# Kernel tuning notes

Measured on AMD Instinct MI355X. Metric: run time of the kernel, lower is better.

The kernel has to match this reference:

```python
import jax, jax.numpy as jnp
import numpy as np

DIM, HID, SEQ = 768, 2048, 4096
LR, MOM, WD, THRESH = 1e-3, 0.9, 0.01, 0.1


def _net(p, x):
    W1, b1, W2, b2, W3, b3, W4, b4 = p
    h = jax.nn.relu(x @ W1 + b1)
    h = jax.nn.relu(h @ W2 + b2)
    h = jax.nn.relu(h @ W3 + b3)
    return h @ W4 + b4


def _loss(p, t):
    # t: [dim]; token.unsqueeze(0) then mse_loss (mean over all elements)
    pred = _net(p, t[None, :])
    return jnp.mean((pred - t[None, :]) ** 2)


def _ttt(params, x):
    toks = x[::4]  # `if i % 4 != 0: continue`

    def step(carry, t):
        p, buf, inited = carry
        g = jax.grad(_loss)(p, t)
        surprise = sum(jnp.linalg.norm(gi) for gi in jax.tree_util.tree_leaves(g))
        # momentum buffer: first observation initializes it
        buf_new = jnp.where(inited, MOM * buf + (1.0 - MOM) * surprise, surprise)

        def upd(q):
            qd = jax.tree_util.tree_map(lambda w: w * (1.0 - WD), q)  # weight decay
            g2 = jax.grad(_loss)(qd, t)                                # fresh fwd/bwd
            return jax.tree_util.tree_map(lambda w, gi: w - LR * gi, qd, g2)  # SGD step

        p_new = jax.lax.cond(buf_new > THRESH, upd, lambda q: q, p)
        return (p_new, buf_new, jnp.bool_(True)), None

    (pf, _, _), _ = jax.lax.scan(step, (params, jnp.float32(0.0), jnp.bool_(False)), toks)
    return pf


def setup_inputs() -> dict:
    key = jax.random.key(0)
    ks = jax.random.split(key, 5)

    def lin(k, fi, fo):
        kw, kb = jax.random.split(k)
        w = jax.random.normal(kw, (fi, fo), jnp.float32) / np.sqrt(fi).astype(np.float32)
        b = jax.random.normal(kb, (fo,), jnp.float32) * 0.01
        return w, b

    W1, b1 = lin(ks[0], DIM, HID)
    W2, b2 = lin(ks[1], HID, HID)
    W3, b3 = lin(ks[2], HID, HID)
    W4, b4 = lin(ks[3], HID, DIM)
    x = jax.random.normal(ks[4], (SEQ, DIM), jnp.float32)
    return dict(x=x, W1=W1, b1=b1, W2=W2, b2=b2, W3=W3, b3=b3, W4=W4, b4=b4, do_ttt=1)


def reference(x, W1, b1, W2, b2, W3, b3, W4, b4, do_ttt):
    params = (W1, b1, W2, b2, W3, b3, W4, b4)
    if do_ttt:
        params = _ttt(params, x)
    out = _net(params, x)            # eval pass over full sequence
    return out.mean(axis=0, keepdims=True)  # memory_summary [1, dim]
```

## Files before the change

### kernel.cpp

```cpp
#include <hip/hip_runtime.h>
#include <cstddef>

#define LRC 0.001f
#define DEC 0.99f

typedef float vf4 __attribute__((ext_vector_type(4)));

static const size_t OFF_Z1T  = 0;
static const size_t OFF_Z2TP = 65536;
static const size_t OFF_Z2TQ = 131072;
static const size_t OFF_Z3TP = 196608;
static const size_t OFF_Z3TQ = 262144;
static const size_t OFF_Z4TP = 327680;
static const size_t OFF_Z4TQ = 352256;
static const size_t OFF_H1F = 376832;
static const size_t OFF_H1Q = 378880;
static const size_t OFF_H2F = 380928;
static const size_t OFF_H2Q = 382976;
static const size_t OFF_H3F = 385024;
static const size_t OFF_H3Q0 = 387072;
static const size_t OFF_D4F = 389120;
static const size_t OFF_D4Q = 389888;
static const size_t OFF_D3F = 390656;
static const size_t OFF_D3Q = 392704;
static const size_t OFF_D2F = 394752;
static const size_t OFF_D2Q = 396800;
static const size_t OFF_D1F = 398848;
static const size_t OFF_D1Q = 400896;
static const size_t OFF_NSQ = 402944;
static const size_t OFF_SL3 = 402960;
static const size_t OFF_SL2 = 403216;
static const size_t OFF_SL1 = 403472;
static const size_t OFF_BUF = 403728;
static const size_t OFF_CONDF = 403730;
static const size_t OFF_MSUM = 403732;
static const size_t OFF_HA  = 428308;
static const size_t OFF_BAR = OFF_HA;
static const size_t OFF_H3Q1 = OFF_HA + 1024;
static const size_t OFF_HB  = 2525460;

struct V8 { vf4 v[8]; };

__device__ __forceinline__ float ld_cv(const float* p) {
    float v;
    asm volatile("global_load_dword %0, %1, off sc0 sc1\n\ts_waitcnt vmcnt(0)"
                 : "=&v"(v) : "v"(p) : "memory");
    return v;
}
__device__ __forceinline__ vf4 ld4_cv(const float* p) {
    vf4 v;
    asm volatile("global_load_dwordx4 %0, %1, off sc0 sc1\n\ts_waitcnt vmcnt(0)"
                 : "=&v"(v) : "v"(p) : "memory");
    return v;
}
__device__ __forceinline__ V8 ld32_cv(const float* p) {
    V8 r;
    asm volatile(
        "global_load_dwordx4 %0, %8, off sc0 sc1\n\t"
        "global_load_dwordx4 %1, %8, off offset:16 sc0 sc1\n\t"
        "global_load_dwordx4 %2, %8, off offset:32 sc0 sc1\n\t"
        "global_load_dwordx4 %3, %8, off offset:48 sc0 sc1\n\t"
        "global_load_dwordx4 %4, %8, off offset:64 sc0 sc1\n\t"
        "global_load_dwordx4 %5, %8, off offset:80 sc0 sc1\n\t"
        "global_load_dwordx4 %6, %8, off offset:96 sc0 sc1\n\t"
        "global_load_dwordx4 %7, %8, off offset:112 sc0 sc1\n\t"
        "s_waitcnt vmcnt(0)"
        : "=&v"(r.v[0]), "=&v"(r.v[1]), "=&v"(r.v[2]), "=&v"(r.v[3]),
          "=&v"(r.v[4]), "=&v"(r.v[5]), "=&v"(r.v[6]), "=&v"(r.v[7])
        : "v"(p) : "memory");
    return r;
}
__device__ __forceinline__ V8 ldrow_cv(const float* p) {
    const float* q = p + 1024;
    V8 r;
    asm volatile(
        "global_load_dwordx4 %0, %8, off sc0 sc1\n\t"
        "global_load_dwordx4 %1, %8, off offset:1024 sc0 sc1\n\t"
        "global_load_dwordx4 %2, %8, off offset:2048 sc0 sc1\n\t"
        "global_load_dwordx4 %3, %8, off offset:3072 sc0 sc1\n\t"
        "global_load_dwordx4 %4, %9, off sc0 sc1\n\t"
        "global_load_dwordx4 %5, %9, off offset:1024 sc0 sc1\n\t"
        "global_load_dwordx4 %6, %9, off offset:2048 sc0 sc1\n\t"
        "global_load_dwordx4 %7, %9, off offset:3072 sc0 sc1\n\t"
        "s_waitcnt vmcnt(0)"
        : "=&v"(r.v[0]), "=&v"(r.v[1]), "=&v"(r.v[2]), "=&v"(r.v[3]),
          "=&v"(r.v[4]), "=&v"(r.v[5]), "=&v"(r.v[6]), "=&v"(r.v[7])
        : "v"(p), "v"(q) : "memory");
    return r;
}
__device__ __forceinline__ void ldrow3_cv(const float* p, vf4& a, vf4& b, vf4& c) {
    asm volatile(
        "global_load_dwordx4 %0, %3, off sc0 sc1\n\t"
        "global_load_dwordx4 %1, %3, off offset:1024 sc0 sc1\n\t"
        "global_load_dwordx4 %2, %3, off offset:2048 sc0 sc1\n\t"
        "s_waitcnt vmcnt(0)"
        : "=&v"(a), "=&v"(b), "=&v"(c) : "v"(p) : "memory");
}
__device__ __forceinline__ void st_cv(float* p, float v) {
    asm volatile("global_store_dword %0, %1, off sc0 sc1" :: "v"(p), "v"(v) : "memory");
}
__device__ __forceinline__ void st_cv4(float* p, vf4 v) {
    asm volatile("global_store_dwordx4 %0, %1, off sc0 sc1" :: "v"(p), "v"(v) : "memory");
}
__device__ __forceinline__ float sum32(const V8& z) {
    float s = 0.f;
#pragma unroll
    for (int i = 0; i < 8; ++i) s += z.v[i].x + z.v[i].y + z.v[i].z + z.v[i].w;
    return s;
}

__device__ float block_reduce_512(float v) {
    __shared__ float red[512];
    int t = threadIdx.x;
    red[t] = v;
    __syncthreads();
    for (int s = 256; s > 0; s >>= 1) {
        if (t < s) red[t] += red[t + s];
        __syncthreads();
    }
    float r = red[0];
    __syncthreads();
    return r;
}

__device__ inline void gbar(int* bar, int bi) {
    asm volatile("s_waitcnt vmcnt(0) lgkmcnt(0)" ::: "memory");
    __syncthreads();
    if (threadIdx.x == 0) {
        int target = bi * 16 + 15;
        int g = (int)(blockIdx.x >> 4);
        int v = __hip_atomic_fetch_add(&bar[g * 16], 1, __ATOMIC_RELAXED, __HIP_MEMORY_SCOPE_AGENT);
        if (v == target) {
            int r = __hip_atomic_fetch_add(&bar[260], 1, __ATOMIC_RELAXED, __HIP_MEMORY_SCOPE_AGENT);
            if (r == target)
                __hip_atomic_store(&bar[276], bi + 1, __ATOMIC_RELAXED, __HIP_MEMORY_SCOPE_AGENT);
        }
        while (__hip_atomic_load(&bar[276], __ATOMIC_RELAXED, __HIP_MEMORY_SCOPE_AGENT) <= bi)
            __builtin_amdgcn_s_sleep(8);
    }
    __syncthreads();
}

__device__ __forceinline__ void fwd2phase(int bblk, int tid, int w, int lane, vf4* s4,
        const float* zinTP, const float* zinTQ, const float* bin,
        float* W, int Nout, float* zoutTP, float* zoutTQ,
        const float* uprev, const float* vprev, float* bl, bool upd) {
    float* sm = (float*)s4;
    float* hs = sm + 4096; float* hq = sm + 4160; float* us = sm + 4224;
    int p = bblk & 31, g = bblk >> 5;
    if (tid < 64) {
        int k = p * 64 + tid;
        V8 zp = ld32_cv(zinTP + (size_t)k * 32);
        float ssum = sum32(zp);
        float bv = ld_cv(bin + k);
        float h = fmaxf(ssum + bv, 0.f);
        float hqq;
        if (zinTQ) {
            V8 zq = ld32_cv(zinTQ + (size_t)k * 32);
            hqq = fmaxf(DEC * (sum32(zq) + bv), 0.f);
        } else {
            hqq = DEC * h;
        }
        hs[tid] = h; hq[tid] = hqq;
        us[tid] = upd ? (LRC * ld_cv(uprev + k)) : 0.f;
    }
    __syncthreads();
    int c0 = g * 256 + lane * 4;
    vf4 vpv = {0.f, 0.f, 0.f, 0.f};
    if (upd) vpv = ld4_cv(vprev + c0);
    vf4 ap = {0.f, 0.f, 0.f, 0.f};
    vf4 aq = {0.f, 0.f, 0.f, 0.f};
    if (upd) {
#pragma unroll
        for (int r = 0; r < 8; ++r) {
            int kk = w * 8 + r;
            float* wp = W + (size_t)(p * 64 + kk) * Nout + c0;
            vf4 wv = *(const vf4*)wp;
            wv = DEC * wv - us[kk] * vpv;
            st_cv4(wp, wv);
            ap += hs[kk] * wv; aq += hq[kk] * wv;
        }
    } else {
#pragma unroll
        for (int r = 0; r < 8; ++r) {
            int kk = w * 8 + r;
            const vf4 wv = *(const vf4*)(W + (size_t)(p * 64 + kk) * Nout + c0);
            ap += hs[kk] * wv; aq += hq[kk] * wv;
        }
    }
    if (upd && bblk == 0) {
        int c = tid * 4;
        if (c < Nout) {
            vf4 dq = ld4_cv(vprev + c);
            vf4 bv = ld4_cv(bl + c);
            st_cv4(bl + c, DEC * bv - LRC * dq);
        }
    }
    s4[w * 64 + lane] = ap;
    s4[512 + w * 64 + lane] = aq;
    __syncthreads();
    if (w == 0) {
        vf4 sp = s4[lane], sq4 = s4[512 + lane];
#pragma unroll
        for (int q = 1; q < 8; ++q) {
            sp += s4[q * 64 + lane];
            sq4 += s4[512 + q * 64 + lane];
        }
        st_cv(zoutTP + (size_t)(c0 + 0) * 32 + p, sp.x);
        st_cv(zoutTP + (size_t)(c0 + 1) * 32 + p, sp.y);
        st_cv(zoutTP + (size_t)(c0 + 2) * 32 + p, sp.z);
        st_cv(zoutTP + (size_t)(c0 + 3) * 32 + p, sp.w);
        st_cv(zoutTQ + (size_t)(c0 + 0) * 32 + p, sq4.x);
        st_cv(zoutTQ + (size_t)(c0 + 1) * 32 + p, sq4.y);
        st_cv(zoutTQ + (size_t)(c0 + 2) * 32 + p, sq4.z);
        st_cv(zoutTQ + (size_t)(c0 + 3) * 32 + p, sq4.w);
    }
}

__device__ __forceinline__ void bwdphase(int bblk, int tid, int w, int lane,
        float* sm, float* sqw, const float* W,
        const float* dinP, const float* dinQ,
        const float* hP, const float* hQ,
        float* doutP, float* doutQ, float* slot) {
    float* dsP = sm; float* dsQ = sm + 2048;
    {
        int k4 = tid * 4;
        vf4 vP = ld4_cv(dinP + k4);
        vf4 vQ = ld4_cv(dinQ + k4);
        *(vf4*)(dsP + k4) = vP;
        *(vf4*)(dsQ + k4) = vQ;
    }
    __syncthreads();
    int j = bblk * 8 + w;
    V8 r = ldrow_cv(W + (size_t)j * 2048 + lane * 4);
    float ap = 0.f, aq = 0.f;
#pragma unroll
    for (int i = 0; i < 8; ++i) {
        int k0 = lane * 4 + i * 256;
        vf4 wv = r.v[i];
        ap += wv.x * dsP[k0] + wv.y * dsP[k0 + 1] + wv.z * dsP[k0 + 2] + wv.w * dsP[k0 + 3];
        aq += wv.x * dsQ[k0] + wv.y * dsQ[k0 + 1] + wv.z * dsQ[k0 + 2] + wv.w * dsQ[k0 + 3];
    }
#pragma unroll
    for (int off = 32; off > 0; off >>= 1) {
        ap += __shfl_down(ap, off);
        aq += __shfl_down(aq, off);
    }
    if (lane == 0) {
        float dp = (ld_cv(hP + j) > 0.f) ? ap : 0.f;
        float dq = (ld_cv(hQ + j) > 0.f) ? DEC * aq : 0.f;
        st_cv(doutP + j, dp); st_cv(doutQ + j, dq); sqw[w] = dp * dp;
    }
    __syncthreads();
    if (tid == 0) {
        float t = 0.f;
#pragma unroll
        for (int q = 0; q < 8; ++q) t += sqw[q];
        st_cv(slot + bblk, t);
    }
}

__global__ __launch_bounds__(512) void k_ttt(const float* __restrict__ x,
        float* __restrict__ W1, float* __restrict__ b1,
        float* __restrict__ W2, float* __restrict__ b2,
        float* __restrict__ W3, float* __restrict__ b3,
        float* __restrict__ W4, float* __restrict__ b4,
        float* __restrict__ wsf, const int* __restrict__ flag, int* __restrict__ bar) {
    if (*flag == 0) return;
    const int b = blockIdx.x, tid = threadIdx.x;
    const int w = tid >> 6, lane = tid & 63;
    __shared__ vf4 s4[1408];
    __shared__ float cnd[12];
    __shared__ float sqw[8];
    __shared__ float updsh;
    float* sm = (float*)s4;
    int bi = 0;

    for (int s = 0; s < 1024; ++s) {
        const float* xt = x + (size_t)s * 3072;
        const float* xp = x + (size_t)(s > 0 ? s - 1 : 0) * 3072;
        float* h3q_cur = wsf + ((s & 1) ? OFF_H3Q1 : OFF_H3Q0);
        const float* h3q_prev = wsf + ((s & 1) ? OFF_H3Q0 : OFF_H3Q1);

        {
            int g = b >> 5, p = b & 31;
            int c0 = g * 256 + lane * 4;
            int kb = p * 24 + w * 3;
            vf4 wv0 = *(const vf4*)(W1 + (size_t)(kb + 0) * 2048 + c0);
            vf4 wv1 = *(const vf4*)(W1 + (size_t)(kb + 1) * 2048 + c0);
            vf4 wv2 = *(const vf4*)(W1 + (size_t)(kb + 2) * 2048 + c0);
            float a0 = xt[kb + 0], a1 = xt[kb + 1], a2 = xt[kb + 2];
            vf4 dv = {0.f, 0.f, 0.f, 0.f};
            float u0 = 0.f, u1 = 0.f, u2 = 0.f;
            float cond = 0.f;
            if (s > 0) {
                dv = ld4_cv(wsf + OFF_D1Q + c0);
                u0 = LRC * xp[kb + 0]; u1 = LRC * xp[kb + 1]; u2 = LRC * xp[kb + 2];
                if (w < 3) {
                    const float* sl = wsf + (w == 0 ? OFF_SL1 : (w == 1 ? OFF_SL2 : OFF_SL3));
                    vf4 v4 = ld4_cv(sl + lane * 4);
                    float v = v4.x + v4.y + v4.z + v4.w;
#pragma unroll
                    for (int off = 32; off > 0; off >>= 1) v += __shfl_down(v, off);
                    if (lane == 0) cnd[w] = v;
                } else if (w == 3 && lane < 6) {
                    cnd[3 + lane] = (lane < 5) ? ld_cv(wsf + OFF_NSQ + lane)
                                               : ld_cv(wsf + OFF_BUF + ((s - 1) & 1));
                }
                __syncthreads();
                float nd1 = sqrtf(cnd[0]), nd2 = sqrtf(cnd[1]), nd3 = sqrtf(cnd[2]);
                float nx = sqrtf(cnd[3]), nh1 = sqrtf(cnd[4]), nh2 = sqrtf(cnd[5]);
                float nh3 = sqrtf(cnd[6]), nd4 = sqrtf(cnd[7]);
                float bufold = cnd[8];
                float surprise = nx * nd1 + nd1 + nh1 * nd2 + nd2 + nh2 * nd3 + nd3 + nh3 * nd4 + nd4;
                float bufnew = (s == 1) ? surprise : (0.9f * bufold + 0.1f * surprise);
                cond = (bufnew > 0.1f) ? 1.f : 0.f;
                if (b == 0 && tid == 0) {
                    st_cv(wsf + OFF_BUF + (s & 1), bufnew);
                    st_cv(wsf + OFF_CONDF, cond);
                }
            } else {
                if (b == 0 && tid == 0) st_cv(wsf + OFF_CONDF, 0.f);
            }
            if (tid == 0) updsh = cond;
            if (cond != 0.f) {
                wv0 = DEC * wv0 - u0 * dv;
                wv1 = DEC * wv1 - u1 * dv;
                wv2 = DEC * wv2 - u2 * dv;
                st_cv4(W1 + (size_t)(kb + 0) * 2048 + c0, wv0);
                st_cv4(W1 + (size_t)(kb + 1) * 2048 + c0, wv1);
                st_cv4(W1 + (size_t)(kb + 2) * 2048 + c0, wv2);
                if (b == 0) {
                    int c = tid * 4;
                    vf4 dq = ld4_cv(wsf + OFF_D1Q + c);
                    vf4 bv = ld4_cv(b1 + c);
                    st_cv4(b1 + c, DEC * bv - LRC * dq);
                }
            }
            vf4 acc = a0 * wv0 + a1 * wv1 + a2 * wv2;
            s4[w * 64 + lane] = acc;
            __syncthreads();
            if (w == 0) {
                vf4 t = s4[lane];
#pragma unroll
                for (int q = 1; q < 8; ++q) t += s4[q * 64 + lane];
                st_cv(wsf + OFF_Z1T + (size_t)(c0 + 0) * 32 + p, t.x);
                st_cv(wsf + OFF_Z1T + (size_t)(c0 + 1) * 32 + p, t.y);
                st_cv(wsf + OFF_Z1T + (size_t)(c0 + 2) * 32 + p, t.z);
                st_cv(wsf + OFF_Z1T + (size_t)(c0 + 3) * 32 + p, t.w);
            }
        }
        gbar(bar, bi++);

        bool upd = (updsh != 0.f);

        fwd2phase(b, tid, w, lane, s4, wsf + OFF_Z1T, nullptr, b1, W2, 2048,
                  wsf + OFF_Z2TP, wsf + OFF_Z2TQ, wsf + OFF_H1Q, wsf + OFF_D2Q, b2, upd);
        gbar(bar, bi++);

        fwd2phase(b, tid, w, lane, s4, wsf + OFF_Z2TP, wsf + OFF_Z2TQ, b2, W3, 2048,
                  wsf + OFF_Z3TP, wsf + OFF_Z3TQ, wsf + OFF_H2Q, wsf + OFF_D3Q, b3, upd);
        gbar(bar, bi++);

        if (b < 96) {
            fwd2phase(b, tid, w, lane, s4, wsf + OFF_Z3TP, wsf + OFF_Z3TQ, b3, W4, 768,
                      wsf + OFF_Z4TP, wsf + OFF_Z4TQ, h3q_prev, wsf + OFF_D4Q, b4, upd);
        } else {
            int idx = b - 96;
            if (idx < 16) {
                if (tid < 128) {
                    int e = idx * 128 + tid;
                    V8 z = ld32_cv(wsf + OFF_Z1T + (size_t)e * 32);
                    float h = fmaxf(sum32(z) + ld_cv(b1 + e), 0.f);
                    st_cv(wsf + OFF_H1F + e, h);
                    st_cv(wsf + OFF_H1Q + e, DEC * h);
                }
            } else if (idx < 32) {
                if (tid < 128) {
                    int e = (idx - 16) * 128 + tid;
                    V8 zp = ld32_cv(wsf + OFF_Z2TP + (size_t)e * 32);
                    V8 zq = ld32_cv(wsf + OFF_Z2TQ + (size_t)e * 32);
                    float bv = ld_cv(b2 + e);
                    st_cv(wsf + OFF_H2F + e, fmaxf(sum32(zp) + bv, 0.f));
                    st_cv(wsf + OFF_H2Q + e, fmaxf(DEC * (sum32(zq) + bv), 0.f));
                }
            } else if (idx < 48) {
                if (tid < 128) {
                    int e = (idx - 32) * 128 + tid;
                    V8 zp = ld32_cv(wsf + OFF_Z3TP + (size_t)e * 32);
                    V8 zq = ld32_cv(wsf + OFF_Z3TQ + (size_t)e * 32);
                    float bv = ld_cv(b3 + e);
                    st_cv(wsf + OFF_H3F + e, fmaxf(sum32(zp) + bv, 0.f));
                    st_cv(h3q_cur + e, fmaxf(DEC * (sum32(zq) + bv), 0.f));
                }
            } else if (idx == 48) {
                float v = 0.f;
                for (int e = tid; e < 768; e += 512) { float xv = xt[e]; v += xv * xv; }
                float t = block_reduce_512(v);
                if (tid == 0) st_cv(wsf + OFF_NSQ + 0, t);
            } else if (idx == 49) {
                float v = 0.f;
                for (int e = tid; e < 2048; e += 512) {
                    V8 z = ld32_cv(wsf + OFF_Z1T + (size_t)e * 32);
                    float h = fmaxf(sum32(z) + ld_cv(b1 + e), 0.f);
                    v += h * h;
                }
                float t = block_reduce_512(v);
                if (tid == 0) st_cv(wsf + OFF_NSQ + 1, t);
            } else if (idx == 50) {
                float v = 0.f;
                for (int e = tid; e < 2048; e += 512) {
                    V8 z = ld32_cv(wsf + OFF_Z2TP + (size_t)e * 32);
                    float h = fmaxf(sum32(z) + ld_cv(b2 + e), 0.f);
                    v += h * h;
                }
                float t = block_reduce_512(v);
                if (tid == 0) st_cv(wsf + OFF_NSQ + 2, t);
            } else if (idx == 51) {
                float v = 0.f;
                for (int e = tid; e < 2048; e += 512) {
                    V8 z = ld32_cv(wsf + OFF_Z3TP + (size_t)e * 32);
                    float h = fmaxf(sum32(z) + ld_cv(b3 + e), 0.f);
                    v += h * h;
                }
                float t = block_reduce_512(v);
                if (tid == 0) st_cv(wsf + OFF_NSQ + 3, t);
            }
        }
        gbar(bar, bi++);

        {
            float* d4P = sm; float* d4Q = sm + 768;
            for (int e = tid; e < 768; e += 512) {
                V8 zp = ld32_cv(wsf + OFF_Z4TP + (size_t)e * 32);
                V8 zq = ld32_cv(wsf + OFF_Z4TQ + (size_t)e * 32);
                float bv = ld_cv(b4 + e), tv = xt[e];
                d4P[e] = 2.f * ((sum32(zp) + bv) - tv) * (1.f / 768.f);
                d4Q[e] = 2.f * (DEC * (sum32(zq) + bv) - tv) * (1.f / 768.f);
            }
            __syncthreads();
            int j = b * 8 + w;
            vf4 r0, r1, r2;
            ldrow3_cv(W4 + (size_t)j * 768 + lane * 4, r0, r1, r2);
            float ap = 0.f, aq = 0.f;
            {
                int k0 = lane * 4;
                ap += r0.x * d4P[k0] + r0.y * d4P[k0 + 1] + r0.z * d4P[k0 + 2] + r0.w * d4P[k0 + 3];
                aq += r0.x * d4Q[k0] + r0.y * d4Q[k0 + 1] + r0.z * d4Q[k0 + 2] + r0.w * d4Q[k0 + 3];
                k0 += 256;
                ap += r1.x * d4P[k0] + r1.y * d4P[k0 + 1] + r1.z * d4P[k0 + 2] + r1.w * d4P[k0 + 3];
                aq += r1.x * d4Q[k0] + r1.y * d4Q[k0 + 1] + r1.z * d4Q[k0 + 2] + r1.w * d4Q[k0 + 3];
                k0 += 256;
                ap += r2.x * d4P[k0] + r2.y * d4P[k0 + 1] + r2.z * d4P[k0 + 2] + r2.w * d4P[k0 + 3];
                aq += r2.x * d4Q[k0] + r2.y * d4Q[k0 + 1] + r2.z * d4Q[k0 + 2] + r2.w * d4Q[k0 + 3];
            }
#pragma unroll
            for (int off = 32; off > 0; off >>= 1) {
                ap += __shfl_down(ap, off);
                aq += __shfl_down(aq, off);
            }
            if (lane == 0) {
                float dp = (ld_cv(wsf + OFF_H3F + j) > 0.f) ? ap : 0.f;
                float dq = (ld_cv(h3q_cur + j) > 0.f) ? DEC * aq : 0.f;
                st_cv(wsf + OFF_D3F + j, dp); st_cv(wsf + OFF_D3Q + j, dq); sqw[w] = dp * dp;
            }
            __syncthreads();
            if (tid == 0) {
                float t = 0.f;
#pragma unroll
                for (int q = 0; q < 8; ++q) t += sqw[q];
                st_cv(wsf + OFF_SL3 + b, t);
            }
            if (b == 0) {
                float v = 0.f;
                for (int e = tid; e < 768; e += 512) {
                    st_cv(wsf + OFF_D4F + e, d4P[e]);
                    st_cv(wsf + OFF_D4Q + e, d4Q[e]);
                    v += d4P[e] * d4P[e];
                }
                float t = block_reduce_512(v);
                if (tid == 0) st_cv(wsf + OFF_NSQ + 4, t);
            }
        }
        gbar(bar, bi++);

        bwdphase(b, tid, w, lane, sm, sqw, W3,
                 wsf + OFF_D3F, wsf + OFF_D3Q, wsf + OFF_H2F, wsf + OFF_H2Q,
                 wsf + OFF_D2F, wsf + OFF_D2Q, wsf + OFF_SL2);
        gbar(bar, bi++);

        bwdphase(b, tid, w, lane, sm, sqw, W2,
                 wsf + OFF_D2F, wsf + OFF_D2Q, wsf + OFF_H1F, wsf + OFF_H1Q,
                 wsf + OFF_D1F, wsf + OFF_D1Q, wsf + OFF_SL1);
        gbar(bar, bi++);
    }
}

__global__ __launch_bounds__(512) void k_upd(int step, float* __restrict__ wsf,
                                             float* __restrict__ W1, float* __restrict__ b1,
                                             float* __restrict__ W2, float* __restrict__ b2,
                                             float* __restrict__ W3, float* __restrict__ b3,
                                             float* __restrict__ W4, float* __restrict__ b4,
                                             const float* __restrict__ xt,
                                             const int* __restrict__ flag) {
    if (*flag == 0) return;
    int tid = threadIdx.x, b = blockIdx.x;
    float s3 = block_reduce_512((tid < 256) ? wsf[OFF_SL3 + tid] : 0.f);
    float s2 = block_reduce_512((tid < 256) ? wsf[OFF_SL2 + tid] : 0.f);
    float s1 = block_reduce_512((tid < 256) ? wsf[OFF_SL1 + tid] : 0.f);
    __shared__ float condsh;
    if (tid == 0) {
        float nx = sqrtf(wsf[OFF_NSQ + 0]);
        float nh1 = sqrtf(wsf[OFF_NSQ + 1]);
        float nh2 = sqrtf(wsf[OFF_NSQ + 2]);
        float nh3 = sqrtf(wsf[OFF_NSQ + 3]);
        float nd4 = sqrtf(wsf[OFF_NSQ + 4]);
        float nd3 = sqrtf(s3), nd2 = sqrtf(s2), nd1 = sqrtf(s1);
        float surprise = nx * nd1 + nd1 + nh1 * nd2 + nd2 + nh2 * nd3 + nd3 + nh3 * nd4 + nd4;
        float bufold = wsf[OFF_BUF + (step & 1)];
        float bufnew = (step == 0) ? surprise : (0.9f * bufold + 0.1f * surprise);
        condsh = (bufnew > 0.1f) ? 1.f : 0.f;
    }
    __syncthreads();
    if (condsh == 0.f) return;

    const float* d1q = wsf + OFF_D1Q;
    const float* d2q = wsf + OFF_D2Q;
    const float* d3q = wsf + OFF_D3Q;
    const float* d4q = wsf + OFF_D4Q;
    const float* h1q = wsf + OFF_H1Q;
    const float* h2q = wsf + OFF_H2Q;
    const float* h3q = wsf + OFF_H3Q1;
    int c = tid * 4;
    {
        float4 dv = *(const float4*)(d1q + c);
#pragma unroll
        for (int r = 0; r < 3; ++r) {
            int i = b * 3 + r;
            float u = LRC * xt[i];
            float4* wp = (float4*)(W1 + (size_t)i * 2048 + c);
            float4 wv = *wp;
            wv.x = DEC * wv.x - u * dv.x; wv.y = DEC * wv.y - u * dv.y;
            wv.z = DEC * wv.z - u * dv.z; wv.w = DEC * wv.w - u * dv.w;
            *wp = wv;
        }
    }
    {
        float4 dv = *(const float4*)(d2q + c);
#pragma unroll
        for (int r = 0; r < 8; ++r) {
            int i = b * 8 + r;
            float u = LRC * h1q[i];
            float4* wp = (float4*)(W2 + (size_t)i * 2048 + c);
            float4 wv = *wp;
            wv.x = DEC * wv.x - u * dv.x; wv.y = DEC * wv.y - u * dv.y;
            wv.z = DEC * wv.z - u * dv.z; wv.w = DEC * wv.w - u * dv.w;
            *wp = wv;
        }
    }
    {
        float4 dv = *(const float4*)(d3q + c);
#pragma unroll
        for (int r = 0; r < 8; ++r) {
            int i = b * 8 + r;
            float u = LRC * h2q[i];
            float4* wp = (float4*)(W3 + (size_t)i * 2048 + c);
            float4 wv = *wp;
            wv.x = DEC * wv.x - u * dv.x; wv.y = DEC * wv.y - u * dv.y;
            wv.z = DEC * wv.z - u * dv.z; wv.w = DEC * wv.w - u * dv.w;
            *wp = wv;
        }
    }
    if (tid < 192) {
        float4 dv = *(const float4*)(d4q + c);
#pragma unroll
        for (int r = 0; r < 8; ++r) {
            int i = b * 8 + r;
            float u = LRC * h3q[i];
            float4* wp = (float4*)(W4 + (size_t)i * 768 + c);
            float4 wv = *wp;
            wv.x = DEC * wv.x - u * dv.x; wv.y = DEC * wv.y - u * dv.y;
            wv.z = DEC * wv.z - u * dv.z; wv.w = DEC * wv.w - u * dv.w;
            *wp = wv;
        }
    }
    if (b == 0) {
        float4 dv = *(const float4*)(d1q + c);
        float4* bp = (float4*)(b1 + c);
        float4 bv = *bp;
        bv.x = DEC * bv.x - LRC * dv.x; bv.y = DEC * bv.y - LRC * dv.y;
        bv.z = DEC * bv.z - LRC * dv.z; bv.w = DEC * bv.w - LRC * dv.w;
        *bp = bv;
    } else if (b == 1) {
        float4 dv = *(const float4*)(d2q + c);
        float4* bp = (float4*)(b2 + c);
        float4 bv = *bp;
        bv.x = DEC * bv.x - LRC * dv.x; bv.y = DEC * bv.y - LRC * dv.y;
        bv.z = DEC * bv.z - LRC * dv.z; bv.w = DEC * bv.w - LRC * dv.w;
        *bp = bv;
    } else if (b == 2) {
        float4 dv = *(const float4*)(d3q + c);
        float4* bp = (float4*)(b3 + c);
        float4 bv = *bp;
        bv.x = DEC * bv.x - LRC * dv.x; bv.y = DEC * bv.y - LRC * dv.y;
        bv.z = DEC * bv.z - LRC * dv.z; bv.w = DEC * bv.w - LRC * dv.w;
        *bp = bv;
    } else if (b == 3 && tid < 192) {
        float4 dv = *(const float4*)(d4q + c);
        float4* bp = (float4*)(b4 + c);
        float4 bv = *bp;
        bv.x = DEC * bv.x - LRC * dv.x; bv.y = DEC * bv.y - LRC * dv.y;
        bv.z = DEC * bv.z - LRC * dv.z; bv.w = DEC * bv.w - LRC * dv.w;
        *bp = bv;
    }
}

__global__ __launch_bounds__(256) void k_gemm(const float* __restrict__ A,
                                              const float* __restrict__ W,
                                              const float* __restrict__ bias,
                                              float* __restrict__ C,
                                              int M, int N, int K, int do_relu) {
    __shared__ float sA[16][64];
    __shared__ float sB[16][128];
    int bn = blockIdx.x, bm = blockIdx.y;
    int m0 = bm * 64, n0 = bn * 128;
    int tid = threadIdx.x;
    int tx = tid & 31, ty = tid >> 5;
    float acc[8][4];
#pragma unroll
    for (int i = 0; i < 8; ++i)
#pragma unroll
        for (int j = 0; j < 4; ++j) acc[i][j] = 0.f;

    for (int kt = 0; kt < K; kt += 16) {
        {
            int r = tid >> 2, cc = (tid & 3) * 4;
            const float4 a4 = *(const float4*)(A + (size_t)(m0 + r) * K + kt + cc);
            sA[cc + 0][r] = a4.x; sA[cc + 1][r] = a4.y; sA[cc + 2][r] = a4.z; sA[cc + 3][r] = a4.w;
        }
        {
            int r = tid >> 5, cc = (tid & 31) * 4;
            *(float4*)(&sB[r][cc]) = *(const float4*)(W + (size_t)(kt + r) * N + n0 + cc);
            *(float4*)(&sB[r + 8][cc]) = *(const float4*)(W + (size_t)(kt + r + 8) * N + n0 + cc);
        }
        __syncthreads();
#pragma unroll
        for (int k = 0; k < 16; ++k) {
            float av[8];
#pragma unroll
            for (int i = 0; i < 8; ++i) av[i] = sA[k][ty * 8 + i];
            float bx = sB[k][tx * 4 + 0], by = sB[k][tx * 4 + 1];
            float bz = sB[k][tx * 4 + 2], bw = sB[k][tx * 4 + 3];
#pragma unroll
            for (int i = 0; i < 8; ++i) {
                acc[i][0] += av[i] * bx; acc[i][1] += av[i] * by;
                acc[i][2] += av[i] * bz; acc[i][3] += av[i] * bw;
            }
        }
        __syncthreads();
    }
    float bx = bias[n0 + tx * 4 + 0], by = bias[n0 + tx * 4 + 1];
    float bz = bias[n0 + tx * 4 + 2], bw = bias[n0 + tx * 4 + 3];
#pragma unroll
    for (int i = 0; i < 8; ++i) {
        int m = m0 + ty * 8 + i;
        float4 v;
        v.x = acc[i][0] + bx; v.y = acc[i][1] + by;
        v.z = acc[i][2] + bz; v.w = acc[i][3] + bw;
        if (do_relu) {
            v.x = fmaxf(v.x, 0.f); v.y = fmaxf(v.y, 0.f);
            v.z = fmaxf(v.z, 0.f); v.w = fmaxf(v.w, 0.f);
        }
        *(float4*)(C + (size_t)m * N + n0 + tx * 4) = v;
    }
}

__global__ __launch_bounds__(128) void k_colsum(const float* __restrict__ Y,
                                                float* __restrict__ out) {
    int c = blockIdx.x * 128 + threadIdx.x;
    int r0 = blockIdx.y * 128;
    float s = 0.f;
    for (int r = 0; r < 128; ++r) s += Y[(size_t)(r0 + r) * 768 + c];
    out[blockIdx.y * 768 + c] = s;
}

__global__ __launch_bounds__(768) void k_out(const float* __restrict__ msum,
                                             float* __restrict__ out) {
    int c = threadIdx.x;
    float s = 0.f;
#pragma unroll
    for (int i = 0; i < 32; ++i) s += msum[i * 768 + c];
    out[c] = s * (1.f / 4096.f);
}

extern "C" void kernel_launch(void* const* d_in, const int* in_sizes, int n_in,
                              void* d_out, int out_size, void* d_ws, size_t ws_size,
                              hipStream_t stream) {
    const float* x = (const float*)d_in[0];
    float* W1 = (float*)d_in[1];
    float* b1 = (float*)d_in[2];
    float* W2 = (float*)d_in[3];
    float* b2 = (float*)d_in[4];
    float* W3 = (float*)d_in[5];
    float* b3 = (float*)d_in[6];
    float* W4 = (float*)d_in[7];
    float* b4 = (float*)d_in[8];
    const int* flag = (const int*)d_in[9];
    float* wsf = (float*)d_ws;
    int* bar = (int*)(wsf + OFF_BAR);

    hipMemsetAsync((void*)bar, 0, 1024 * sizeof(int), stream);

    void* args[] = {(void*)&x, (void*)&W1, (void*)&b1, (void*)&W2, (void*)&b2,
                    (void*)&W3, (void*)&b3, (void*)&W4, (void*)&b4,
                    (void*)&wsf, (void*)&flag, (void*)&bar};
    hipLaunchCooperativeKernel((void*)k_ttt, dim3(256), dim3(512), args, 0, stream);

    k_upd<<<256, 512, 0, stream>>>(1023, wsf, W1, b1, W2, b2, W3, b3, W4, b4,
                                   x + (size_t)1023 * 4 * 768, flag);

    float* HA = wsf + OFF_HA;
    float* HB = wsf + OFF_HB;
    for (int ch = 0; ch < 4; ++ch) {
        const float* Xc = x + (size_t)ch * 1024 * 768;
        k_gemm<<<dim3(16, 16), 256, 0, stream>>>(Xc, W1, b1, HA, 1024, 2048, 768, 1);
        k_gemm<<<dim3(16, 16), 256, 0, stream>>>(HA, W2, b2, HB, 1024, 2048, 2048, 1);
        k_gemm<<<dim3(16, 16), 256, 0, stream>>>(HB, W3, b3, HA, 1024, 2048, 2048, 1);
        k_gemm<<<dim3(6, 16), 256, 0, stream>>>(HA, W4, b4, HB, 1024, 768, 2048, 0);
        k_colsum<<<dim3(6, 8), 128, 0, stream>>>(HB, wsf + OFF_MSUM + (size_t)ch * 8 * 768);
    }
    k_out<<<1, 768, 0, stream>>>(wsf + OFF_MSUM, (float*)d_out);
}
```

Baseline: 72.48 ms.

## Batch coherent loads under one wait and spread z-transpose reductions across threads

Splits the coherent load helpers into issue and wait parts, so each phase issues all of its global loads together and then waits once, instead of waiting on every load in turn. The per-element 32-wide partial-sum reads of the transposed activations are spread across 8 (or 4) threads per element, with the reduction finished in shared memory, rather than one thread reading 32 floats serially. Also shortens the spin-barrier sleep and adds a two-blocks-per-CU launch bound. This trades larger shared memory use and extra syncthreads for more memory-level parallelism in the latency-bound persistent kernel.

```diff
diff --git a/kernel.cpp b/kernel.cpp
--- a/kernel.cpp
+++ b/kernel.cpp
@@ -39,40 +39,26 @@
 static const size_t OFF_H3Q1 = OFF_HA + 1024;
 static const size_t OFF_HB  = 2525460;
 
-struct V8 { vf4 v[8]; };
-
+#define PIN(v) asm volatile("" : "+v"(v))
+__device__ __forceinline__ void vmwait() { asm volatile("s_waitcnt vmcnt(0)" ::: "memory"); }
+__device__ __forceinline__ float ld_nw(const float* p) {
+    float v;
+    asm volatile("global_load_dword %0, %1, off sc0 sc1" : "=&v"(v) : "v"(p) : "memory");
+    return v;
+}
+__device__ __forceinline__ vf4 ld4_nw(const float* p) {
+    vf4 v;
+    asm volatile("global_load_dwordx4 %0, %1, off sc0 sc1" : "=&v"(v) : "v"(p) : "memory");
+    return v;
+}
 __device__ __forceinline__ float ld_cv(const float* p) {
-    float v;
-    asm volatile("global_load_dword %0, %1, off sc0 sc1\n\ts_waitcnt vmcnt(0)"
-                 : "=&v"(v) : "v"(p) : "memory");
-    return v;
+    float v = ld_nw(p); vmwait(); PIN(v); return v;
 }
 __device__ __forceinline__ vf4 ld4_cv(const float* p) {
-    vf4 v;
-    asm volatile("global_load_dwordx4 %0, %1, off sc0 sc1\n\ts_waitcnt vmcnt(0)"
-                 : "=&v"(v) : "v"(p) : "memory");
-    return v;
-}
-__device__ __forceinline__ V8 ld32_cv(const float* p) {
-    V8 r;
-    asm volatile(
-        "global_load_dwordx4 %0, %8, off sc0 sc1\n\t"
-        "global_load_dwordx4 %1, %8, off offset:16 sc0 sc1\n\t"
-        "global_load_dwordx4 %2, %8, off offset:32 sc0 sc1\n\t"
-        "global_load_dwordx4 %3, %8, off offset:48 sc0 sc1\n\t"
-        "global_load_dwordx4 %4, %8, off offset:64 sc0 sc1\n\t"
-        "global_load_dwordx4 %5, %8, off offset:80 sc0 sc1\n\t"
-        "global_load_dwordx4 %6, %8, off offset:96 sc0 sc1\n\t"
-        "global_load_dwordx4 %7, %8, off offset:112 sc0 sc1\n\t"
-        "s_waitcnt vmcnt(0)"
-        : "=&v"(r.v[0]), "=&v"(r.v[1]), "=&v"(r.v[2]), "=&v"(r.v[3]),
-          "=&v"(r.v[4]), "=&v"(r.v[5]), "=&v"(r.v[6]), "=&v"(r.v[7])
-        : "v"(p) : "memory");
-    return r;
-}
-__device__ __forceinline__ V8 ldrow_cv(const float* p) {
+    vf4 v = ld4_nw(p); vmwait(); PIN(v); return v;
+}
+__device__ __forceinline__ void ldrow_nw(const float* p, vf4* r) {
     const float* q = p + 1024;
-    V8 r;
     asm volatile(
         "global_load_dwordx4 %0, %8, off sc0 sc1\n\t"
         "global_load_dwordx4 %1, %8, off offset:1024 sc0 sc1\n\t"
@@ -81,19 +67,16 @@
         "global_load_dwordx4 %4, %9, off sc0 sc1\n\t"
         "global_load_dwordx4 %5, %9, off offset:1024 sc0 sc1\n\t"
         "global_load_dwordx4 %6, %9, off offset:2048 sc0 sc1\n\t"
-        "global_load_dwordx4 %7, %9, off offset:3072 sc0 sc1\n\t"
-        "s_waitcnt vmcnt(0)"
-        : "=&v"(r.v[0]), "=&v"(r.v[1]), "=&v"(r.v[2]), "=&v"(r.v[3]),
-          "=&v"(r.v[4]), "=&v"(r.v[5]), "=&v"(r.v[6]), "=&v"(r.v[7])
+        "global_load_dwordx4 %7, %9, off offset:3072 sc0 sc1"
+        : "=&v"(r[0]), "=&v"(r[1]), "=&v"(r[2]), "=&v"(r[3]),
+          "=&v"(r[4]), "=&v"(r[5]), "=&v"(r[6]), "=&v"(r[7])
         : "v"(p), "v"(q) : "memory");
-    return r;
-}
-__device__ __forceinline__ void ldrow3_cv(const float* p, vf4& a, vf4& b, vf4& c) {
+}
+__device__ __forceinline__ void ldrow3_nw(const float* p, vf4& a, vf4& b, vf4& c) {
     asm volatile(
         "global_load_dwordx4 %0, %3, off sc0 sc1\n\t"
         "global_load_dwordx4 %1, %3, off offset:1024 sc0 sc1\n\t"
-        "global_load_dwordx4 %2, %3, off offset:2048 sc0 sc1\n\t"
-        "s_waitcnt vmcnt(0)"
+        "global_load_dwordx4 %2, %3, off offset:2048 sc0 sc1"
         : "=&v"(a), "=&v"(b), "=&v"(c) : "v"(p) : "memory");
 }
 __device__ __forceinline__ void st_cv(float* p, float v) {
@@ -102,12 +85,7 @@
 __device__ __forceinline__ void st_cv4(float* p, vf4 v) {
     asm volatile("global_store_dwordx4 %0, %1, off sc0 sc1" :: "v"(p), "v"(v) : "memory");
 }
-__device__ __forceinline__ float sum32(const V8& z) {
-    float s = 0.f;
-#pragma unroll
-    for (int i = 0; i < 8; ++i) s += z.v[i].x + z.v[i].y + z.v[i].z + z.v[i].w;
-    return s;
-}
+__device__ __forceinline__ float sum4(vf4 v) { return v.x + v.y + v.z + v.w; }
 
 __device__ float block_reduce_512(float v) {
     __shared__ float red[512];
@@ -136,56 +114,82 @@
                 __hip_atomic_store(&bar[276], bi + 1, __ATOMIC_RELAXED, __HIP_MEMORY_SCOPE_AGENT);
         }
         while (__hip_atomic_load(&bar[276], __ATOMIC_RELAXED, __HIP_MEMORY_SCOPE_AGENT) <= bi)
-            __builtin_amdgcn_s_sleep(8);
-    }
-    __syncthreads();
-}
-
-__device__ __forceinline__ void fwd2phase(int bblk, int tid, int w, int lane, vf4* s4,
+            __builtin_amdgcn_s_sleep(4);
+    }
+    __syncthreads();
+}
+
+__device__ __forceinline__ void fwd2phase(int bblk, int tid, int w, int lane, float* SM,
         const float* zinTP, const float* zinTQ, const float* bin,
         float* W, int Nout, float* zoutTP, float* zoutTQ,
         const float* uprev, const float* vprev, float* bl, bool upd) {
-    float* sm = (float*)s4;
-    float* hs = sm + 4096; float* hq = sm + 4160; float* us = sm + 4224;
+    vf4* s4 = (vf4*)SM;
+    float* hP8   = SM + 6144;
+    float* hQ8   = SM + 6656;
+    float* biasL = SM + 7168;
+    float* usL   = SM + 7232;
+    float* hsL   = SM + 7296;
+    float* hqL   = SM + 7360;
     int p = bblk & 31, g = bblk >> 5;
+    int kb = p * 64;
+    int kk = tid >> 3, ch = tid & 7;
+    int c0 = g * 256 + lane * 4;
+    bool hasQ = (zinTQ != nullptr);
+
+    vf4 zp = ld4_nw(zinTP + (size_t)(kb + kk) * 32 + ch * 4);
+    vf4 zq;
+    if (hasQ) zq = ld4_nw(zinTQ + (size_t)(kb + kk) * 32 + ch * 4);
+    vf4 bi4; if (tid < 16) bi4 = ld4_nw(bin + kb + tid * 4);
+    vf4 uu4; if (upd && tid >= 16 && tid < 32) uu4 = ld4_nw(uprev + kb + (tid - 16) * 4);
+    vf4 vpv; if (upd) vpv = ld4_nw(vprev + c0);
+    vmwait();
+    PIN(zp); if (hasQ) PIN(zq);
+    if (tid < 16) PIN(bi4);
+    if (upd && tid >= 16 && tid < 32) PIN(uu4);
+    if (upd) PIN(vpv);
+
+    hP8[kk * 8 + ch] = sum4(zp);
+    if (hasQ) hQ8[kk * 8 + ch] = sum4(zq);
+    if (tid < 16) *(vf4*)(biasL + tid * 4) = bi4;
+    if (upd && tid >= 16 && tid < 32) *(vf4*)(usL + (tid - 16) * 4) = LRC * uu4;
+    __syncthreads();
     if (tid < 64) {
-        int k = p * 64 + tid;
-        V8 zp = ld32_cv(zinTP + (size_t)k * 32);
-        float ssum = sum32(zp);
-        float bv = ld_cv(bin + k);
-        float h = fmaxf(ssum + bv, 0.f);
-        float hqq;
-        if (zinTQ) {
-            V8 zq = ld32_cv(zinTQ + (size_t)k * 32);
-            hqq = fmaxf(DEC * (sum32(zq) + bv), 0.f);
+        float s = 0.f;
+#pragma unroll
+        for (int c = 0; c < 8; ++c) s += hP8[tid * 8 + c];
+        float bv = biasL[tid];
+        float h = fmaxf(s + bv, 0.f);
+        float hq;
+        if (hasQ) {
+            float sq = 0.f;
+#pragma unroll
+            for (int c = 0; c < 8; ++c) sq += hQ8[tid * 8 + c];
+            hq = fmaxf(DEC * (sq + bv), 0.f);
         } else {
-            hqq = DEC * h;
-        }
-        hs[tid] = h; hq[tid] = hqq;
-        us[tid] = upd ? (LRC * ld_cv(uprev + k)) : 0.f;
-    }
-    __syncthreads();
-    int c0 = g * 256 + lane * 4;
-    vf4 vpv = {0.f, 0.f, 0.f, 0.f};
-    if (upd) vpv = ld4_cv(vprev + c0);
+            hq = DEC * h;
+        }
+        hsL[tid] = h; hqL[tid] = hq;
+    }
+    __syncthreads();
+
     vf4 ap = {0.f, 0.f, 0.f, 0.f};
     vf4 aq = {0.f, 0.f, 0.f, 0.f};
     if (upd) {
 #pragma unroll
         for (int r = 0; r < 8; ++r) {
-            int kk = w * 8 + r;
-            float* wp = W + (size_t)(p * 64 + kk) * Nout + c0;
+            int k2 = w * 8 + r;
+            float* wp = W + (size_t)(p * 64 + k2) * Nout + c0;
             vf4 wv = *(const vf4*)wp;
-            wv = DEC * wv - us[kk] * vpv;
+            wv = DEC * wv - usL[k2] * vpv;
             st_cv4(wp, wv);
-            ap += hs[kk] * wv; aq += hq[kk] * wv;
+            ap += hsL[k2] * wv; aq += hqL[k2] * wv;
         }
     } else {
 #pragma unroll
         for (int r = 0; r < 8; ++r) {
-            int kk = w * 8 + r;
-            const vf4 wv = *(const vf4*)(W + (size_t)(p * 64 + kk) * Nout + c0);
-            ap += hs[kk] * wv; aq += hq[kk] * wv;
+            int k2 = w * 8 + r;
+            const vf4 wv = *(const vf4*)(W + (size_t)(p * 64 + k2) * Nout + c0);
+            ap += hsL[k2] * wv; aq += hqL[k2] * wv;
         }
     }
     if (upd && bblk == 0) {
@@ -202,10 +206,7 @@
     if (w == 0) {
         vf4 sp = s4[lane], sq4 = s4[512 + lane];
 #pragma unroll
-        for (int q = 1; q < 8; ++q) {
-            sp += s4[q * 64 + lane];
-            sq4 += s4[512 + q * 64 + lane];
-        }
+        for (int q = 1; q < 8; ++q) { sp += s4[q * 64 + lane]; sq4 += s4[512 + q * 64 + lane]; }
         st_cv(zoutTP + (size_t)(c0 + 0) * 32 + p, sp.x);
         st_cv(zoutTP + (size_t)(c0 + 1) * 32 + p, sp.y);
         st_cv(zoutTP + (size_t)(c0 + 2) * 32 + p, sp.z);
@@ -218,26 +219,32 @@
 }
 
 __device__ __forceinline__ void bwdphase(int bblk, int tid, int w, int lane,
-        float* sm, float* sqw, const float* W,
+        float* SM, float* sqw, const float* W,
         const float* dinP, const float* dinQ,
         const float* hP, const float* hQ,
         float* doutP, float* doutQ, float* slot) {
-    float* dsP = sm; float* dsQ = sm + 2048;
-    {
-        int k4 = tid * 4;
-        vf4 vP = ld4_cv(dinP + k4);
-        vf4 vQ = ld4_cv(dinQ + k4);
-        *(vf4*)(dsP + k4) = vP;
-        *(vf4*)(dsQ + k4) = vQ;
-    }
-    __syncthreads();
+    float* dsP = SM; float* dsQ = SM + 2048;
+    int k4 = tid * 4;
+    vf4 vP = ld4_nw(dinP + k4);
+    vf4 vQ = ld4_nw(dinQ + k4);
     int j = bblk * 8 + w;
-    V8 r = ldrow_cv(W + (size_t)j * 2048 + lane * 4);
+    vf4 r[8];
+    ldrow_nw(W + (size_t)j * 2048 + lane * 4, r);
+    float gP, gQ;
+    if (lane == 0) { gP = ld_nw(hP + j); gQ = ld_nw(hQ + j); }
+    vmwait();
+    PIN(vP); PIN(vQ);
+#pragma unroll
+    for (int i = 0; i < 8; ++i) PIN(r[i]);
+    if (lane == 0) { PIN(gP); PIN(gQ); }
+    *(vf4*)(dsP + k4) = vP;
+    *(vf4*)(dsQ + k4) = vQ;
+    __syncthreads();
     float ap = 0.f, aq = 0.f;
 #pragma unroll
     for (int i = 0; i < 8; ++i) {
         int k0 = lane * 4 + i * 256;
-        vf4 wv = r.v[i];
+        vf4 wv = r[i];
         ap += wv.x * dsP[k0] + wv.y * dsP[k0 + 1] + wv.z * dsP[k0 + 2] + wv.w * dsP[k0 + 3];
         aq += wv.x * dsQ[k0] + wv.y * dsQ[k0 + 1] + wv.z * dsQ[k0 + 2] + wv.w * dsQ[k0 + 3];
     }
@@ -247,8 +254,8 @@
         aq += __shfl_down(aq, off);
     }
     if (lane == 0) {
-        float dp = (ld_cv(hP + j) > 0.f) ? ap : 0.f;
-        float dq = (ld_cv(hQ + j) > 0.f) ? DEC * aq : 0.f;
+        float dp = (gP > 0.f) ? ap : 0.f;
+        float dq = (gQ > 0.f) ? DEC * aq : 0.f;
         st_cv(doutP + j, dp); st_cv(doutQ + j, dq); sqw[w] = dp * dp;
     }
     __syncthreads();
@@ -260,7 +267,7 @@
     }
 }
 
-__global__ __launch_bounds__(512) void k_ttt(const float* __restrict__ x,
+__global__ __launch_bounds__(512, 2) void k_ttt(const float* __restrict__ x,
         float* __restrict__ W1, float* __restrict__ b1,
         float* __restrict__ W2, float* __restrict__ b2,
         float* __restrict__ W3, float* __restrict__ b3,
@@ -269,11 +276,9 @@
     if (*flag == 0) return;
     const int b = blockIdx.x, tid = threadIdx.x;
     const int w = tid >> 6, lane = tid & 63;
-    __shared__ vf4 s4[1408];
+    __shared__ float SM[14592];
     __shared__ float cnd[12];
     __shared__ float sqw[8];
-    __shared__ float updsh;
-    float* sm = (float*)s4;
     int bi = 0;
 
     for (int s = 0; s < 1024; ++s) {
@@ -281,8 +286,10 @@
         const float* xp = x + (size_t)(s > 0 ? s - 1 : 0) * 3072;
         float* h3q_cur = wsf + ((s & 1) ? OFF_H3Q1 : OFF_H3Q0);
         const float* h3q_prev = wsf + ((s & 1) ? OFF_H3Q0 : OFF_H3Q1);
+        float cond = 0.f;
 
         {
+            vf4* s4 = (vf4*)SM;
             int g = b >> 5, p = b & 31;
             int c0 = g * 256 + lane * 4;
             int kb = p * 24 + w * 3;
@@ -292,20 +299,28 @@
             float a0 = xt[kb + 0], a1 = xt[kb + 1], a2 = xt[kb + 2];
             vf4 dv = {0.f, 0.f, 0.f, 0.f};
             float u0 = 0.f, u1 = 0.f, u2 = 0.f;
-            float cond = 0.f;
             if (s > 0) {
-                dv = ld4_cv(wsf + OFF_D1Q + c0);
+                dv = ld4_nw(wsf + OFF_D1Q + c0);
+                vf4 sl4;
+                if (w < 3) {
+                    const float* sl = wsf + (w == 0 ? OFF_SL1 : (w == 1 ? OFF_SL2 : OFF_SL3));
+                    sl4 = ld4_nw(sl + lane * 4);
+                }
+                float nv;
+                if (w == 3 && lane < 6)
+                    nv = ld_nw(lane < 5 ? (wsf + OFF_NSQ + lane) : (wsf + OFF_BUF + ((s - 1) & 1)));
+                vmwait();
+                PIN(dv);
+                if (w < 3) PIN(sl4);
+                if (w == 3 && lane < 6) PIN(nv);
                 u0 = LRC * xp[kb + 0]; u1 = LRC * xp[kb + 1]; u2 = LRC * xp[kb + 2];
                 if (w < 3) {
-                    const float* sl = wsf + (w == 0 ? OFF_SL1 : (w == 1 ? OFF_SL2 : OFF_SL3));
-                    vf4 v4 = ld4_cv(sl + lane * 4);
-                    float v = v4.x + v4.y + v4.z + v4.w;
+                    float v = sum4(sl4);
 #pragma unroll
                     for (int off = 32; off > 0; off >>= 1) v += __shfl_down(v, off);
                     if (lane == 0) cnd[w] = v;
                 } else if (w == 3 && lane < 6) {
-                    cnd[3 + lane] = (lane < 5) ? ld_cv(wsf + OFF_NSQ + lane)
-                                               : ld_cv(wsf + OFF_BUF + ((s - 1) & 1));
+                    cnd[3 + lane] = nv;
                 }
                 __syncthreads();
                 float nd1 = sqrtf(cnd[0]), nd2 = sqrtf(cnd[1]), nd3 = sqrtf(cnd[2]);
@@ -322,7 +337,6 @@
             } else {
                 if (b == 0 && tid == 0) st_cv(wsf + OFF_CONDF, 0.f);
             }
-            if (tid == 0) updsh = cond;
             if (cond != 0.f) {
                 wv0 = DEC * wv0 - u0 * dv;
                 wv1 = DEC * wv1 - u1 * dv;
@@ -351,97 +365,146 @@
             }
         }
         gbar(bar, bi++);
-
-        bool upd = (updsh != 0.f);
-
-        fwd2phase(b, tid, w, lane, s4, wsf + OFF_Z1T, nullptr, b1, W2, 2048,
+        bool upd = (cond != 0.f);
+
+        fwd2phase(b, tid, w, lane, SM, wsf + OFF_Z1T, nullptr, b1, W2, 2048,
                   wsf + OFF_Z2TP, wsf + OFF_Z2TQ, wsf + OFF_H1Q, wsf + OFF_D2Q, b2, upd);
         gbar(bar, bi++);
 
-        fwd2phase(b, tid, w, lane, s4, wsf + OFF_Z2TP, wsf + OFF_Z2TQ, b2, W3, 2048,
+        fwd2phase(b, tid, w, lane, SM, wsf + OFF_Z2TP, wsf + OFF_Z2TQ, b2, W3, 2048,
                   wsf + OFF_Z3TP, wsf + OFF_Z3TQ, wsf + OFF_H2Q, wsf + OFF_D3Q, b3, upd);
         gbar(bar, bi++);
 
         if (b < 96) {
-            fwd2phase(b, tid, w, lane, s4, wsf + OFF_Z3TP, wsf + OFF_Z3TQ, b3, W4, 768,
+            fwd2phase(b, tid, w, lane, SM, wsf + OFF_Z3TP, wsf + OFF_Z3TQ, b3, W4, 768,
                       wsf + OFF_Z4TP, wsf + OFF_Z4TQ, h3q_prev, wsf + OFF_D4Q, b4, upd);
         } else {
             int idx = b - 96;
+            float* partP = SM;
+            float* partQ = SM + 512;
+            float* biasD = SM + 1024;
             if (idx < 16) {
+                int base = idx * 128, el = tid >> 2, c2 = tid & 3;
+                const float* zl = wsf + OFF_Z1T + (size_t)(base + el) * 32 + c2 * 8;
+                vf4 za = ld4_nw(zl), zb = ld4_nw(zl + 4);
+                vf4 bb; if (tid < 32) bb = ld4_nw(b1 + base + tid * 4);
+                vmwait(); PIN(za); PIN(zb); if (tid < 32) PIN(bb);
+                partP[el * 4 + c2] = sum4(za) + sum4(zb);
+                if (tid < 32) *(vf4*)(biasD + tid * 4) = bb;
+                __syncthreads();
                 if (tid < 128) {
-                    int e = idx * 128 + tid;
-                    V8 z = ld32_cv(wsf + OFF_Z1T + (size_t)e * 32);
-                    float h = fmaxf(sum32(z) + ld_cv(b1 + e), 0.f);
-                    st_cv(wsf + OFF_H1F + e, h);
-                    st_cv(wsf + OFF_H1Q + e, DEC * h);
-                }
-            } else if (idx < 32) {
+                    float sv = partP[tid * 4] + partP[tid * 4 + 1] + partP[tid * 4 + 2] + partP[tid * 4 + 3];
+                    float h = fmaxf(sv + biasD[tid], 0.f);
+                    st_cv(wsf + OFF_H1F + base + tid, h);
+                    st_cv(wsf + OFF_H1Q + base + tid, DEC * h);
+                }
+            } else if (idx < 48) {
+                int l3 = (idx >= 32);
+                int base = (idx - (l3 ? 32 : 16)) * 128, el = tid >> 2, c2 = tid & 3;
+                const float* ZP = wsf + (l3 ? OFF_Z3TP : OFF_Z2TP);
+                const float* ZQ = wsf + (l3 ? OFF_Z3TQ : OFF_Z2TQ);
+                const float* bb_ = l3 ? b3 : b2;
+                const float* zp0 = ZP + (size_t)(base + el) * 32 + c2 * 8;
+                const float* zq0 = ZQ + (size_t)(base + el) * 32 + c2 * 8;
+                vf4 pa = ld4_nw(zp0), pb = ld4_nw(zp0 + 4);
+                vf4 qa = ld4_nw(zq0), qb = ld4_nw(zq0 + 4);
+                vf4 bb; if (tid < 32) bb = ld4_nw(bb_ + base + tid * 4);
+                vmwait(); PIN(pa); PIN(pb); PIN(qa); PIN(qb); if (tid < 32) PIN(bb);
+                partP[el * 4 + c2] = sum4(pa) + sum4(pb);
+                partQ[el * 4 + c2] = sum4(qa) + sum4(qb);
+                if (tid < 32) *(vf4*)(biasD + tid * 4) = bb;
+                __syncthreads();
                 if (tid < 128) {
-                    int e = (idx - 16) * 128 + tid;
-                    V8 zp = ld32_cv(wsf + OFF_Z2TP + (size_t)e * 32);
-                    V8 zq = ld32_cv(wsf + OFF_Z2TQ + (size_t)e * 32);
-                    float bv = ld_cv(b2 + e);
-                    st_cv(wsf + OFF_H2F + e, fmaxf(sum32(zp) + bv, 0.f));
-                    st_cv(wsf + OFF_H2Q + e, fmaxf(DEC * (sum32(zq) + bv), 0.f));
-                }
-            } else if (idx < 48) {
-                if (tid < 128) {
-                    int e = (idx - 32) * 128 + tid;
-                    V8 zp = ld32_cv(wsf + OFF_Z3TP + (size_t)e * 32);
-                    V8 zq = ld32_cv(wsf + OFF_Z3TQ + (size_t)e * 32);
-                    float bv = ld_cv(b3 + e);
-                    st_cv(wsf + OFF_H3F + e, fmaxf(sum32(zp) + bv, 0.f));
-                    st_cv(h3q_cur + e, fmaxf(DEC * (sum32(zq) + bv), 0.f));
+                    float sp = partP[tid * 4] + partP[tid * 4 + 1] + partP[tid * 4 + 2] + partP[tid * 4 + 3];
+                    float sq = partQ[tid * 4] + partQ[tid * 4 + 1] + partQ[tid * 4 + 2] + partQ[tid * 4 + 3];
+                    float bv = biasD[tid];
+                    if (l3) {
+                        st_cv(wsf + OFF_H3F + base + tid, fmaxf(sp + bv, 0.f));
+                        st_cv(h3q_cur + base + tid, fmaxf(DEC * (sq + bv), 0.f));
+                    } else {
+                        st_cv(wsf + OFF_H2F + base + tid, fmaxf(sp + bv, 0.f));
+                        st_cv(wsf + OFF_H2Q + base + tid, fmaxf(DEC * (sq + bv), 0.f));
+                    }
                 }
             } else if (idx == 48) {
                 float v = 0.f;
                 for (int e = tid; e < 768; e += 512) { float xv = xt[e]; v += xv * xv; }
                 float t = block_reduce_512(v);
                 if (tid == 0) st_cv(wsf + OFF_NSQ + 0, t);
-            } else if (idx == 49) {
-                float v = 0.f;
-                for (int e = tid; e < 2048; e += 512) {
-                    V8 z = ld32_cv(wsf + OFF_Z1T + (size_t)e * 32);
-                    float h = fmaxf(sum32(z) + ld_cv(b1 + e), 0.f);
-                    v += h * h;
-                }
-                float t = block_reduce_512(v);
-                if (tid == 0) st_cv(wsf + OFF_NSQ + 1, t);
-            } else if (idx == 50) {
-                float v = 0.f;
-                for (int e = tid; e < 2048; e += 512) {
-                    V8 z = ld32_cv(wsf + OFF_Z2TP + (size_t)e * 32);
-                    float h = fmaxf(sum32(z) + ld_cv(b2 + e), 0.f);
-                    v += h * h;
-                }
-                float t = block_reduce_512(v);
-                if (tid == 0) st_cv(wsf + OFF_NSQ + 2, t);
-            } else if (idx == 51) {
-                float v = 0.f;
-                for (int e = tid; e < 2048; e += 512) {
-                    V8 z = ld32_cv(wsf + OFF_Z3TP + (size_t)e * 32);
-                    float h = fmaxf(sum32(z) + ld_cv(b3 + e), 0.f);
-                    v += h * h;
-                }
-                float t = block_reduce_512(v);
-                if (tid == 0) st_cv(wsf + OFF_NSQ + 3, t);
+            } else if (idx < 52) {
+                const float* ZT = (idx == 49) ? (wsf + OFF_Z1T) : (idx == 50 ? (wsf + OFF_Z2TP) : (wsf + OFF_Z3TP));
+                const float* bb_ = (idx == 49) ? b1 : (idx == 50 ? b2 : b3);
+                int nk = idx - 48;
+                float acc = 0.f;
+#pragma unroll
+                for (int pass = 0; pass < 4; ++pass) {
+                    int e = pass * 512 + tid;
+                    const float* zl = ZT + (size_t)e * 32;
+                    vf4 z0 = ld4_nw(zl), z1 = ld4_nw(zl + 4), z2 = ld4_nw(zl + 8), z3 = ld4_nw(zl + 12);
+                    vf4 z4 = ld4_nw(zl + 16), z5 = ld4_nw(zl + 20), z6 = ld4_nw(zl + 24), z7 = ld4_nw(zl + 28);
+                    float bv = ld_nw(bb_ + e);
+                    vmwait();
+                    PIN(z0); PIN(z1); PIN(z2); PIN(z3); PIN(z4); PIN(z5); PIN(z6); PIN(z7); PIN(bv);
+                    float sv = sum4(z0) + sum4(z1) + sum4(z2) + sum4(z3)
+                             + sum4(z4) + sum4(z5) + sum4(z6) + sum4(z7);
+                    float h = fmaxf(sv + bv, 0.f);
+                    acc += h * h;
+                }
+                float t = block_reduce_512(acc);
+                if (tid == 0) st_cv(wsf + OFF_NSQ + nk, t);
             }
         }
         gbar(bar, bi++);
 
         {
-            float* d4P = sm; float* d4Q = sm + 768;
-            for (int e = tid; e < 768; e += 512) {
-                V8 zp = ld32_cv(wsf + OFF_Z4TP + (size_t)e * 32);
-                V8 zq = ld32_cv(wsf + OFF_Z4TQ + (size_t)e * 32);
-                float bv = ld_cv(b4 + e), tv = xt[e];
-                d4P[e] = 2.f * ((sum32(zp) + bv) - tv) * (1.f / 768.f);
-                d4Q[e] = 2.f * (DEC * (sum32(zq) + bv) - tv) * (1.f / 768.f);
-            }
-            __syncthreads();
+            float* partP = SM;
+            float* partQ = SM + 6144;
+            float* d4P   = SM + 12288;
+            float* d4Q   = SM + 13056;
+            float* biasE = SM + 13824;
+            int er = tid >> 3, ch = tid & 7;
+            vf4 pv[12];
+#pragma unroll
+            for (int i = 0; i < 12; ++i)
+                pv[i] = ld4_nw(wsf + OFF_Z4TP + (size_t)(i * 64 + er) * 32 + ch * 4);
+            vf4 b4v; if (tid < 192) b4v = ld4_nw(b4 + tid * 4);
+            vmwait();
+#pragma unroll
+            for (int i = 0; i < 12; ++i) PIN(pv[i]);
+            if (tid < 192) PIN(b4v);
+#pragma unroll
+            for (int i = 0; i < 12; ++i) partP[(size_t)(i * 64 + er) * 8 + ch] = sum4(pv[i]);
+            if (tid < 192) *(vf4*)(biasE + tid * 4) = b4v;
+            vf4 qv[12];
+#pragma unroll
+            for (int i = 0; i < 12; ++i)
+                qv[i] = ld4_nw(wsf + OFF_Z4TQ + (size_t)(i * 64 + er) * 32 + ch * 4);
             int j = b * 8 + w;
             vf4 r0, r1, r2;
-            ldrow3_cv(W4 + (size_t)j * 768 + lane * 4, r0, r1, r2);
+            ldrow3_nw(W4 + (size_t)j * 768 + lane * 4, r0, r1, r2);
+            float gP, gQ;
+            if (lane == 0) { gP = ld_nw(wsf + OFF_H3F + j); gQ = ld_nw(h3q_cur + j); }
+            vmwait();
+#pragma unroll
+            for (int i = 0; i < 12; ++i) PIN(qv[i]);
+            PIN(r0); PIN(r1); PIN(r2);
+            if (lane == 0) { PIN(gP); PIN(gQ); }
+#pragma unroll
+            for (int i = 0; i < 12; ++i) partQ[(size_t)(i * 64 + er) * 8 + ch] = sum4(qv[i]);
+            __syncthreads();
+            if (tid < 256) {
+#pragma unroll
+                for (int m = 0; m < 3; ++m) {
+                    int e = tid + m * 256;
+                    float sp = 0.f, sq = 0.f;
+#pragma unroll
+                    for (int c = 0; c < 8; ++c) { sp += partP[e * 8 + c]; sq += partQ[e * 8 + c]; }
+                    float bv = biasE[e], tv = xt[e];
+                    d4P[e] = 2.f * ((sp + bv) - tv) * (1.f / 768.f);
+                    d4Q[e] = 2.f * (DEC * (sq + bv) - tv) * (1.f / 768.f);
+                }
+            }
+            __syncthreads();
             float ap = 0.f, aq = 0.f;
             {
                 int k0 = lane * 4;
@@ -460,8 +523,8 @@
                 aq += __shfl_down(aq, off);
             }
             if (lane == 0) {
-                float dp = (ld_cv(wsf + OFF_H3F + j) > 0.f) ? ap : 0.f;
-                float dq = (ld_cv(h3q_cur + j) > 0.f) ? DEC * aq : 0.f;
+                float dp = (gP > 0.f) ? ap : 0.f;
+                float dq = (gQ > 0.f) ? DEC * aq : 0.f;
                 st_cv(wsf + OFF_D3F + j, dp); st_cv(wsf + OFF_D3Q + j, dq); sqw[w] = dp * dp;
             }
             __syncthreads();
@@ -484,12 +547,12 @@
         }
         gbar(bar, bi++);
 
-        bwdphase(b, tid, w, lane, sm, sqw, W3,
+        bwdphase(b, tid, w, lane, SM, sqw, W3,
                  wsf + OFF_D3F, wsf + OFF_D3Q, wsf + OFF_H2F, wsf + OFF_H2Q,
                  wsf + OFF_D2F, wsf + OFF_D2Q, wsf + OFF_SL2);
         gbar(bar, bi++);
 
-        bwdphase(b, tid, w, lane, sm, sqw, W2,
+        bwdphase(b, tid, w, lane, SM, sqw, W2,
                  wsf + OFF_D2F, wsf + OFF_D2Q, wsf + OFF_H1F, wsf + OFF_H1Q,
                  wsf + OFF_D1F, wsf + OFF_D1Q, wsf + OFF_SL1);
         gbar(bar, bi++);
```

Result: slower. 77.57 ms (+7.0%).
